# Kernel tuning notes

Measured on AMD Instinct MI355X. Metric: run time of the kernel, lower is better.

Reference implementation:

```python
import jax, jax.numpy as jnp
import numpy as np

B, N, C, H = 2, 2048, 1024, 16
D = C // H  # head_dim = 64


def _rope_freqs(n, d_half, theta=10000.0):
    inv = 1.0 / (theta ** (np.arange(0, d_half, dtype=np.float32) / d_half))
    ang = np.arange(n, dtype=np.float32)[:, None] * inv[None, :]
    return jnp.asarray(np.cos(ang)), jnp.asarray(np.sin(ang))


def setup_inputs() -> dict:
    key = jax.random.key(0)
    ks = jax.random.split(key, 5)
    cos, sin = _rope_freqs(N, D // 2)
    s = 0.02
    return {
        "x": jax.random.normal(ks[0], (B, N, C), jnp.float32),
        "w_qkv": jax.random.normal(ks[1], (3 * C, C), jnp.float32) * s,
        "b_qkv": jnp.zeros((3 * C,), jnp.float32),
        "w_proj": jax.random.normal(ks[2], (C, C), jnp.float32) * s,
        "b_proj": jnp.zeros((C,), jnp.float32),
        "freqs_cos": cos,
        "freqs_sin": sin,
    }


def _apply_rope(t, cos, sin):
    # t: (B, H, N, D); consecutive pairs (even, odd) form complex numbers,
    # matching torch.view_as_complex on reshape(..., D//2, 2).
    te = t[..., 0::2]
    to = t[..., 1::2]
    cos = cos[None, None, :, :]  # (1,1,N,D//2)
    sin = sin[None, None, :, :]
    oe = te * cos - to * sin
    oo = te * sin + to * cos
    return jnp.stack([oe, oo], axis=-1).reshape(t.shape)


def reference(x, w_qkv, b_qkv, w_proj, b_proj, freqs_cos, freqs_sin):
    b, n, c = x.shape
    qkv = x @ w_qkv.T + b_qkv                      # (B,N,3C)
    qkv = qkv.reshape(b, n, 3, H, D).transpose(2, 0, 3, 1, 4)  # (3,B,H,N,D)
    q, k, v = qkv[0], qkv[1], qkv[2]
    q = _apply_rope(q, freqs_cos, freqs_sin)
    k = _apply_rope(k, freqs_cos, freqs_sin)
    scale = 1.0 / jnp.sqrt(jnp.asarray(D, x.dtype))
    scores = jnp.einsum("bhqd,bhkd->bhqk", q, k) * scale
    attn = jax.nn.softmax(scores, axis=-1)
    out = jnp.einsum("bhqk,bhkd->bhqd", attn, v)   # (B,H,N,D)
    out = out.transpose(0, 2, 1, 3).reshape(b, n, c)
    return out @ w_proj.T + b_proj
```

## Files before the change

kernel.cpp:

```cpp
#include <hip/hip_runtime.h>
#include <hip/hip_bf16.h>
#include <stdint.h>

#define BB 2
#define NN 2048
#define CC 1024
#define HH 16
#define DD 64
#define C3 3072

typedef __attribute__((ext_vector_type(8))) short bf16x8;
typedef __attribute__((ext_vector_type(4))) short bf16x4;
typedef __attribute__((ext_vector_type(4))) float f32x4;
typedef __attribute__((ext_vector_type(16))) float f32x16;
typedef __attribute__((ext_vector_type(4))) unsigned short ushort4_t;

__device__ __forceinline__ unsigned short f2bf(float f) {
  union { float f; unsigned u; } v; v.f = f;
  unsigned r = v.u + 0x7FFFu + ((v.u >> 16) & 1u);
  return (unsigned short)(r >> 16);
}

#if __has_builtin(__builtin_amdgcn_exp2f)
#define EXP2(x) __builtin_amdgcn_exp2f(x)
#else
#define EXP2(x) exp2f(x)
#endif

__device__ __forceinline__ unsigned pack_bf2(float a, float b) {
  union { float f; unsigned u; } ua, ub; ua.f = a; ub.f = b;
#if __has_builtin(__builtin_amdgcn_perm)
  return __builtin_amdgcn_perm(ub.u, ua.u, 0x07060302u);
#else
  return (ua.u >> 16) | (ub.u & 0xFFFF0000u);
#endif
}

#define QSCALE 0.18033688f

#define GLDS(g, l) __builtin_amdgcn_global_load_lds( \
    (const __attribute__((address_space(1))) void*)(g), \
    (__attribute__((address_space(3))) void*)(l), 16, 0, 0)

__global__ __launch_bounds__(256) void k_cvt(
    const float* __restrict__ x, const float* __restrict__ wq,
    const float* __restrict__ wp,
    unsigned short* __restrict__ xb, unsigned short* __restrict__ wqb,
    unsigned short* __restrict__ wpb)
{
  int blk = blockIdx.x;
  const float* s; unsigned short* d; int i;
  if (blk < 4096)      { s = x;  d = xb;  i = blk * 256 + threadIdx.x; }
  else if (blk < 7168) { s = wq; d = wqb; i = (blk - 4096) * 256 + threadIdx.x; }
  else                 { s = wp; d = wpb; i = (blk - 7168) * 256 + threadIdx.x; }
  float4 v = ((const float4*)s)[i];
  ushort4_t o;
  o.x = f2bf(v.x); o.y = f2bf(v.y); o.z = f2bf(v.z); o.w = f2bf(v.w);
  ((ushort4_t*)d)[i] = o;
}

__global__ __launch_bounds__(256) void k_gemm_qkv(
    const unsigned short* __restrict__ A, const unsigned short* __restrict__ Bt,
    const float* __restrict__ bias,
    const float* __restrict__ cosb, const float* __restrict__ sinb,
    unsigned short* __restrict__ Qg, unsigned short* __restrict__ Kg,
    unsigned short* __restrict__ Vt)
{
  __shared__ __align__(16) unsigned short Sh[16384];
  const int tid  = threadIdx.x;
  const int lane = tid & 63;
  const int wave = tid >> 6;
  const int bm = blockIdx.y * 128;
  const int bn = blockIdx.x * 128;
  const int wm = (wave >> 1) * 64;
  const int wn = (wave & 1) * 64;
  const int frow = lane & 15;
  const int fk   = (lane >> 4) * 8;
  const int K = 1024;
  const int NIT = K / 32;

  f32x4 acc[4][4] = {};

  const int row0 = tid >> 2, cc0 = tid & 3;
  const int row1 = row0 + 64;
  const unsigned short* Arow0 = A  + (size_t)(bm + row0) * K + cc0 * 8;
  const unsigned short* Arow1 = A  + (size_t)(bm + row1) * K + cc0 * 8;
  const unsigned short* Brow0 = Bt + (size_t)(bn + row0) * K + cc0 * 8;
  const unsigned short* Brow1 = Bt + (size_t)(bn + row1) * K + cc0 * 8;

  GLDS(Arow0, Sh + (size_t)tid * 8);
  GLDS(Brow0, Sh + 4096 + (size_t)tid * 8);
  GLDS(Arow1, Sh + (size_t)(tid + 256) * 8);
  GLDS(Brow1, Sh + 4096 + (size_t)(tid + 256) * 8);

  for (int it = 0; it < NIT; ++it) {
    const int p = it & 1;
    const unsigned short* As = Sh + p * 8192;
    const unsigned short* Bs = As + 4096;
    __syncthreads();

    if (it + 1 < NIT) {
      const int k1 = (it + 1) * 32;
      unsigned short* An = Sh + (1 - p) * 8192;
      GLDS(Arow0 + k1, An + (size_t)tid * 8);
      GLDS(Brow0 + k1, An + 4096 + (size_t)tid * 8);
      GLDS(Arow1 + k1, An + (size_t)(tid + 256) * 8);
      GLDS(Brow1 + k1, An + 4096 + (size_t)(tid + 256) * 8);
    }

    bf16x8 af[4], bfr[4];
#pragma unroll
    for (int t = 0; t < 4; ++t) {
      af[t]  = *(const bf16x8*)(As + (wm + t * 16 + frow) * 32 + fk);
      bfr[t] = *(const bf16x8*)(Bs + (wn + t * 16 + frow) * 32 + fk);
    }
#pragma unroll
    for (int mt = 0; mt < 4; ++mt)
#pragma unroll
      for (int nt = 0; nt < 4; ++nt)
        acc[mt][nt] = __builtin_amdgcn_mfma_f32_16x16x32_bf16(af[mt], bfr[nt], acc[mt][nt], 0, 0, 0);
  }
  __syncthreads();

  const int er0  = (lane >> 4) * 4;
  const int ecol = lane & 15;
  const int region = bn >> 10;
  const int gcol0 = bn + wn;
  const int h  = (gcol0 >> 6) & 15;
  const int rowg0 = bm + wm;
  const int b  = rowg0 >> 11;
  const int n0 = rowg0 & (NN - 1);
  unsigned short* wt = Sh + wave * 4096;

#pragma unroll
  for (int nt = 0; nt < 4; ++nt) {
    const int c64 = nt * 16 + ecol;
    const float bv = bias[gcol0 + c64];
    const int ii  = c64 >> 1;
#pragma unroll
    for (int mt = 0; mt < 4; ++mt)
#pragma unroll
      for (int r = 0; r < 4; ++r) {
        const int ml = mt * 16 + er0 + r;
        const int n  = n0 + ml;
        float v = acc[mt][nt][r] + bv;
        float vp = __shfl_xor(v, 1, 64);
        if (region == 2) {
          wt[c64 * 64 + ((((ml >> 3) ^ (c64 & 7)) << 3) | (ml & 7))] = f2bf(v);
        } else {
          float cth = cosb[n * 32 + ii], sth = sinb[n * 32 + ii];
          float ov = (c64 & 1) ? (vp * sth + v * cth)
                               : (v * cth - vp * sth);
          if (region == 0) ov *= QSCALE;
          wt[ml * 64 + ((((c64 >> 3) ^ (ml & 7)) << 3) | (c64 & 7))] = f2bf(ov);
        }
      }
  }

  const int rr = lane >> 3, cc = lane & 7;
  if (region == 2) {
    unsigned short* dst = Vt + (size_t)(b * HH + h) * DD * NN + n0;
#pragma unroll
    for (int it = 0; it < 8; ++it) {
      int dl = it * 8 + rr;
      bf16x8 vv = *(const bf16x8*)(wt + dl * 64 + ((cc ^ (dl & 7)) << 3));
      *(bf16x8*)(dst + (size_t)dl * NN + cc * 8) = vv;
    }
  } else {
    unsigned short* dqk = ((region == 0) ? Qg : Kg) +
                          ((size_t)(b * HH + h) * NN + n0) * DD;
#pragma unroll
    for (int it = 0; it < 8; ++it) {
      int ml = it * 8 + rr;
      bf16x8 vv = *(const bf16x8*)(wt + ml * 64 + ((cc ^ (ml & 7)) << 3));
      *(bf16x8*)(dqk + (size_t)ml * DD + cc * 8) = vv;
    }
  }
}

__global__ __launch_bounds__(256) void k_attn(
    const unsigned short* __restrict__ Qg, const unsigned short* __restrict__ Kg,
    const unsigned short* __restrict__ Vtg, unsigned short* __restrict__ Og)
{
  __shared__ __align__(16) unsigned short Ks[2][64 * 64];
  __shared__ __align__(16) unsigned short Vs[2][64 * 64];

  const int tid  = threadIdx.x;
  const int lane = tid & 63;
  const int wave = tid >> 6;
  const int bh = blockIdx.x >> 4;
  const int qt = blockIdx.x & 15;
  const int q0 = qt * 128 + wave * 32;
  const int l31 = lane & 31;
  const int hi  = lane >> 5;
  const int s7  = l31 & 7;

  const unsigned short* Qb = Qg  + (size_t)bh * NN * DD;
  const unsigned short* Kb = Kg  + (size_t)bh * NN * DD;
  const unsigned short* Vb = Vtg + (size_t)bh * DD * NN;

  int koff[4];
#pragma unroll
  for (int x = 0; x < 4; ++x)
    koff[x] = l31 * 64 + (((2 * x + hi) ^ s7) << 3);

  int vkoff[8];
#pragma unroll
  for (int c = 0; c < 8; ++c)
    vkoff[c] = l31 * 64 + ((c ^ s7) << 3) + hi * 4;

  bf16x8 qf[4];
#pragma unroll
  for (int dc = 0; dc < 4; ++dc)
    qf[dc] = *(const bf16x8*)(Qb + (size_t)(q0 + l31) * DD + dc * 16 + hi * 8);

  f32x16 oacc[2] = {};
  float lsum = 0.f;

  const int row0 = tid >> 3, cc0 = tid & 7;
  const int sw0 = (cc0 ^ (row0 & 7)) * 8;

  GLDS(Kb + (size_t)row0 * DD + sw0,        Ks[0] + (size_t)tid * 8);
  GLDS(Vb + (size_t)row0 * NN + sw0,        Vs[0] + (size_t)tid * 8);
  GLDS(Kb + (size_t)(row0 + 32) * DD + sw0, Ks[0] + (size_t)(tid + 256) * 8);
  GLDS(Vb + (size_t)(row0 + 32) * NN + sw0, Vs[0] + (size_t)(tid + 256) * 8);

  for (int t = 0; t < NN / 64; ++t) {
    const int p = t & 1;
    const unsigned short* Kp = Ks[p];
    const unsigned short* Vp = Vs[p];
    __syncthreads();

    if (t + 1 < NN / 64) {
      const int j = (t + 1) * 64;
      GLDS(Kb + (size_t)(j + row0) * DD + sw0,      Ks[1 - p] + (size_t)tid * 8);
      GLDS(Vb + (size_t)row0 * NN + j + sw0,        Vs[1 - p] + (size_t)tid * 8);
      GLDS(Kb + (size_t)(j + row0 + 32) * DD + sw0, Ks[1 - p] + (size_t)(tid + 256) * 8);
      GLDS(Vb + (size_t)(row0 + 32) * NN + j + sw0, Vs[1 - p] + (size_t)(tid + 256) * 8);
    }

    f32x16 sacc[2] = {};
#pragma unroll
    for (int T = 0; T < 2; ++T)
#pragma unroll
      for (int dc = 0; dc < 4; ++dc) {
        bf16x8 kf = *(const bf16x8*)(Kp + T * 2048 + koff[dc]);
        sacc[T] = __builtin_amdgcn_mfma_f32_32x32x16_bf16(kf, qf[dc], sacc[T], 0, 0, 0);
      }

#pragma unroll
    for (int T = 0; T < 2; ++T) {
      unsigned pk[8];
#pragma unroll
      for (int jj = 0; jj < 8; ++jj) {
        float e0 = EXP2(sacc[T][2 * jj]);
        float e1 = EXP2(sacc[T][2 * jj + 1]);
        lsum += e0 + e1;
        pk[jj] = pack_bf2(e0, e1);
      }
      union { unsigned u[4]; bf16x8 v; } fa, fb;
      fa.u[0] = pk[0]; fa.u[1] = pk[1]; fa.u[2] = pk[2]; fa.u[3] = pk[3];
      fb.u[0] = pk[4]; fb.u[1] = pk[5]; fb.u[2] = pk[6]; fb.u[3] = pk[7];
#pragma unroll
      for (int dt = 0; dt < 2; ++dt) {
        union { bf16x4 h[2]; bf16x8 w; } v0, v1;
        v0.h[0] = *(const bf16x4*)(Vp + dt * 2048 + vkoff[4 * T + 0]);
        v0.h[1] = *(const bf16x4*)(Vp + dt * 2048 + vkoff[4 * T + 1]);
        v1.h[0] = *(const bf16x4*)(Vp + dt * 2048 + vkoff[4 * T + 2]);
        v1.h[1] = *(const bf16x4*)(Vp + dt * 2048 + vkoff[4 * T + 3]);
        oacc[dt] = __builtin_amdgcn_mfma_f32_32x32x16_bf16(fa.v, v0.w, oacc[dt], 0, 0, 0);
        oacc[dt] = __builtin_amdgcn_mfma_f32_32x32x16_bf16(fb.v, v1.w, oacc[dt], 0, 0, 0);
      }
    }
  }

  float ltot = lsum + __shfl_xor(lsum, 32, 64);
  const int b = bh >> 4;
  const int h = bh & 15;
#pragma unroll
  for (int r = 0; r < 16; ++r) {
    const int qr = (r & 3) + 8 * (r >> 2) + 4 * hi;
    const float linv = 1.0f / __shfl(ltot, qr, 64);
    unsigned short* orow = Og + (size_t)(b * NN + q0 + qr) * CC + h * DD + l31;
    orow[0]  = f2bf(oacc[0][r] * linv);
    orow[32] = f2bf(oacc[1][r] * linv);
  }
}

__global__ __launch_bounds__(256) void k_gemm_proj(
    const unsigned short* __restrict__ A, const unsigned short* __restrict__ Bt,
    const float* __restrict__ bias, float* __restrict__ Co)
{
  __shared__ __align__(16) unsigned short As[2][64 * 32];
  __shared__ __align__(16) unsigned short Bs[2][128 * 32];
  const int tid  = threadIdx.x;
  const int lane = tid & 63;
  const int wave = tid >> 6;
  const int bm = blockIdx.y * 64;
  const int bn = blockIdx.x * 128;
  const int wm = (wave >> 1) * 32;
  const int wn = (wave & 1) * 64;
  const int frow = lane & 15;
  const int fk   = (lane >> 4) * 8;
  const int K = 1024;
  const int NIT = K / 32;

  f32x4 acc[2][4] = {};

  const int row0 = tid >> 2, cc0 = tid & 3;
  const unsigned short* Arow  = A  + (size_t)(bm + row0) * K + cc0 * 8;
  const unsigned short* Brow0 = Bt + (size_t)(bn + row0) * K + cc0 * 8;
  const unsigned short* Brow1 = Bt + (size_t)(bn + row0 + 64) * K + cc0 * 8;

  GLDS(Arow,  As[0] + (size_t)tid * 8);
  GLDS(Brow0, Bs[0] + (size_t)tid * 8);
  GLDS(Brow1, Bs[0] + (size_t)(tid + 256) * 8);

  for (int it = 0; it < NIT; ++it) {
    const int p = it & 1;
    __syncthreads();

    if (it + 1 < NIT) {
      const int k1 = (it + 1) * 32;
      GLDS(Arow  + k1, As[1 - p] + (size_t)tid * 8);
      GLDS(Brow0 + k1, Bs[1 - p] + (size_t)tid * 8);
      GLDS(Brow1 + k1, Bs[1 - p] + (size_t)(tid + 256) * 8);
    }

    bf16x8 af[2], bfr[4];
#pragma unroll
    for (int t = 0; t < 2; ++t)
      af[t] = *(const bf16x8*)(As[p] + (wm + t * 16 + frow) * 32 + fk);
#pragma unroll
    for (int t = 0; t < 4; ++t)
      bfr[t] = *(const bf16x8*)(Bs[p] + (wn + t * 16 + frow) * 32 + fk);
#pragma unroll
    for (int mt = 0; mt < 2; ++mt)
#pragma unroll
      for (int nt = 0; nt < 4; ++nt)
        acc[mt][nt] = __builtin_amdgcn_mfma_f32_16x16x32_bf16(af[mt], bfr[nt], acc[mt][nt], 0, 0, 0);
  }

  const int er0  = (lane >> 4) * 4;
  const int ecol = lane & 15;
#pragma unroll
  for (int nt = 0; nt < 4; ++nt) {
    int col = bn + wn + nt * 16 + ecol;
    float bv = bias[col];
#pragma unroll
    for (int mt = 0; mt < 2; ++mt)
#pragma unroll
      for (int r = 0; r < 4; ++r) {
        int rowg = bm + wm + mt * 16 + er0 + r;
        Co[(size_t)rowg * CC + col] = acc[mt][nt][r] + bv;
      }
  }
}

extern "C" void kernel_launch(void* const* d_in, const int* in_sizes, int n_in,
                              void* d_out, int out_size, void* d_ws, size_t ws_size,
                              hipStream_t stream)
{
  const float* x      = (const float*)d_in[0];
  const float* w_qkv  = (const float*)d_in[1];
  const float* b_qkv  = (const float*)d_in[2];
  const float* w_proj = (const float*)d_in[3];
  const float* b_proj = (const float*)d_in[4];
  const float* fcos   = (const float*)d_in[5];
  const float* fsin   = (const float*)d_in[6];
  float* out = (float*)d_out;

  char* ws = (char*)d_ws;
  unsigned short* xb     = (unsigned short*)(ws);
  unsigned short* wqkvb  = (unsigned short*)(ws + 8388608);
  unsigned short* wprojb = (unsigned short*)(ws + 14680064);
  unsigned short* Qb     = (unsigned short*)(ws + 16777216);
  unsigned short* Kb     = (unsigned short*)(ws + 25165824);
  unsigned short* Vtb    = (unsigned short*)(ws + 33554432);
  unsigned short* aob    = (unsigned short*)(ws + 41943040);

  k_cvt<<<8192, 256, 0, stream>>>(x, w_qkv, w_proj, xb, wqkvb, wprojb);

  k_gemm_qkv<<<dim3(24, 32), 256, 0, stream>>>(xb, wqkvb, b_qkv, fcos, fsin,
                                               Qb, Kb, Vtb);

  k_attn<<<512, 256, 0, stream>>>(Qb, Kb, Vtb, aob);

  k_gemm_proj<<<dim3(8, 64), 256, 0, stream>>>(aob, wprojb, b_proj, out);
}
```

Before: 202.5 us.

## Compute softmax row sums via MFMA with ones and permute V layout for 16-byte LDS reads

The Vt layout written by the QKV kernel is permuted so the attention kernel can load each V fragment with single 16-byte LDS reads instead of paired 8-byte reads, and it now shares one offset table with K. The softmax denominator is accumulated by extra MFMAs against a ones vector instead of scalar adds plus shuffles, which removes VALU work from the exp loop. The loop also gets s_setprio around the MFMA sections and an unroll of 2 with byte-offset addressing. The trade-off is two extra MFMAs per tile, an extra 16-register accumulator and bf16-rounded probabilities feeding the sum.

```diff
diff --git a/kernel.cpp b/kernel.cpp
--- a/kernel.cpp
+++ b/kernel.cpp
@@ -160,11 +160,16 @@
   const int rr = lane >> 3, cc = lane & 7;
   if (region == 2) {
     unsigned short* dst = Vt + (size_t)(b * HH + h) * DD * NN + n0;
+    const int q8a = (cc >> 1) * 2;
+    const int q8b = q8a + 1;
+    const int half = (cc & 1) * 4;
 #pragma unroll
     for (int it = 0; it < 8; ++it) {
       int dl = it * 8 + rr;
-      bf16x8 vv = *(const bf16x8*)(wt + dl * 64 + ((cc ^ (dl & 7)) << 3));
-      *(bf16x8*)(dst + (size_t)dl * NN + cc * 8) = vv;
+      union { bf16x4 h[2]; bf16x8 w; } vv;
+      vv.h[0] = *(const bf16x4*)(wt + dl * 64 + ((q8a ^ (dl & 7)) << 3) + half);
+      vv.h[1] = *(const bf16x4*)(wt + dl * 64 + ((q8b ^ (dl & 7)) << 3) + half);
+      *(bf16x8*)(dst + (size_t)dl * NN + cc * 8) = vv.w;
     }
   } else {
     unsigned short* dqk = ((region == 0) ? Qg : Kg) +
@@ -199,23 +204,24 @@
   const unsigned short* Kb = Kg  + (size_t)bh * NN * DD;
   const unsigned short* Vb = Vtg + (size_t)bh * DD * NN;
 
-  int koff[4];
-#pragma unroll
-  for (int x = 0; x < 4; ++x)
-    koff[x] = l31 * 64 + (((2 * x + hi) ^ s7) << 3);
-
-  int vkoff[8];
-#pragma unroll
-  for (int c = 0; c < 8; ++c)
-    vkoff[c] = l31 * 64 + ((c ^ s7) << 3) + hi * 4;
+  int soffB[4];
+#pragma unroll
+  for (int i = 0; i < 4; ++i)
+    soffB[i] = (l31 * 64 + (((2 * i + hi) ^ s7) << 3)) * 2;
+  const char* KsB = (const char*)Ks;
+  const char* VsB = (const char*)Vs;
 
   bf16x8 qf[4];
 #pragma unroll
   for (int dc = 0; dc < 4; ++dc)
     qf[dc] = *(const bf16x8*)(Qb + (size_t)(q0 + l31) * DD + dc * 16 + hi * 8);
 
+  bf16x8 ones;
+#pragma unroll
+  for (int i = 0; i < 8; ++i) ones[i] = (short)0x3F80;
+
   f32x16 oacc[2] = {};
-  float lsum = 0.f;
+  f32x16 lacc = {};
 
   const int row0 = tid >> 3, cc0 = tid & 7;
   const int sw0 = (cc0 ^ (row0 & 7)) * 8;
@@ -225,10 +231,9 @@
   GLDS(Kb + (size_t)(row0 + 32) * DD + sw0, Ks[0] + (size_t)(tid + 256) * 8);
   GLDS(Vb + (size_t)(row0 + 32) * NN + sw0, Vs[0] + (size_t)(tid + 256) * 8);
 
+#pragma unroll 2
   for (int t = 0; t < NN / 64; ++t) {
     const int p = t & 1;
-    const unsigned short* Kp = Ks[p];
-    const unsigned short* Vp = Vs[p];
     __syncthreads();
 
     if (t + 1 < NN / 64) {
@@ -240,13 +245,15 @@
     }
 
     f32x16 sacc[2] = {};
+    __builtin_amdgcn_s_setprio(1);
 #pragma unroll
     for (int T = 0; T < 2; ++T)
 #pragma unroll
       for (int dc = 0; dc < 4; ++dc) {
-        bf16x8 kf = *(const bf16x8*)(Kp + T * 2048 + koff[dc]);
+        bf16x8 kf = *(const bf16x8*)(KsB + p * 8192 + T * 4096 + soffB[dc]);
         sacc[T] = __builtin_amdgcn_mfma_f32_32x32x16_bf16(kf, qf[dc], sacc[T], 0, 0, 0);
       }
+    __builtin_amdgcn_s_setprio(0);
 
 #pragma unroll
     for (int T = 0; T < 2; ++T) {
@@ -255,32 +262,31 @@
       for (int jj = 0; jj < 8; ++jj) {
         float e0 = EXP2(sacc[T][2 * jj]);
         float e1 = EXP2(sacc[T][2 * jj + 1]);
-        lsum += e0 + e1;
         pk[jj] = pack_bf2(e0, e1);
       }
       union { unsigned u[4]; bf16x8 v; } fa, fb;
       fa.u[0] = pk[0]; fa.u[1] = pk[1]; fa.u[2] = pk[2]; fa.u[3] = pk[3];
       fb.u[0] = pk[4]; fb.u[1] = pk[5]; fb.u[2] = pk[6]; fb.u[3] = pk[7];
+      __builtin_amdgcn_s_setprio(1);
 #pragma unroll
       for (int dt = 0; dt < 2; ++dt) {
-        union { bf16x4 h[2]; bf16x8 w; } v0, v1;
-        v0.h[0] = *(const bf16x4*)(Vp + dt * 2048 + vkoff[4 * T + 0]);
-        v0.h[1] = *(const bf16x4*)(Vp + dt * 2048 + vkoff[4 * T + 1]);
-        v1.h[0] = *(const bf16x4*)(Vp + dt * 2048 + vkoff[4 * T + 2]);
-        v1.h[1] = *(const bf16x4*)(Vp + dt * 2048 + vkoff[4 * T + 3]);
-        oacc[dt] = __builtin_amdgcn_mfma_f32_32x32x16_bf16(fa.v, v0.w, oacc[dt], 0, 0, 0);
-        oacc[dt] = __builtin_amdgcn_mfma_f32_32x32x16_bf16(fb.v, v1.w, oacc[dt], 0, 0, 0);
-      }
-    }
-  }
-
-  float ltot = lsum + __shfl_xor(lsum, 32, 64);
+        bf16x8 v0 = *(const bf16x8*)(VsB + p * 8192 + dt * 4096 + soffB[2 * T + 0]);
+        bf16x8 v1 = *(const bf16x8*)(VsB + p * 8192 + dt * 4096 + soffB[2 * T + 1]);
+        oacc[dt] = __builtin_amdgcn_mfma_f32_32x32x16_bf16(fa.v, v0, oacc[dt], 0, 0, 0);
+        oacc[dt] = __builtin_amdgcn_mfma_f32_32x32x16_bf16(fb.v, v1, oacc[dt], 0, 0, 0);
+      }
+      lacc = __builtin_amdgcn_mfma_f32_32x32x16_bf16(fa.v, ones, lacc, 0, 0, 0);
+      lacc = __builtin_amdgcn_mfma_f32_32x32x16_bf16(fb.v, ones, lacc, 0, 0, 0);
+      __builtin_amdgcn_s_setprio(0);
+    }
+  }
+
   const int b = bh >> 4;
   const int h = bh & 15;
 #pragma unroll
   for (int r = 0; r < 16; ++r) {
     const int qr = (r & 3) + 8 * (r >> 2) + 4 * hi;
-    const float linv = 1.0f / __shfl(ltot, qr, 64);
+    const float linv = 1.0f / lacc[r];
     unsigned short* orow = Og + (size_t)(b * NN + q0 + qr) * CC + h * DD + l31;
     orow[0]  = f2bf(oacc[0][r] * linv);
     orow[32] = f2bf(oacc[1][r] * linv);
```

New measurement: 200.8 us. About the same (-0.8%).
